# Performance work log

Measured on AMD Instinct MI355X. Metric: run time of the kernel, lower is better.

## Reference

```python
import jax, jax.numpy as jnp
import numpy as np

B, N, K, F_IN, F_OUT = 2, 196608, 9, 64, 64


def setup_inputs() -> dict:
    key = jax.random.key(0)
    k1, k2, k3 = jax.random.split(key, 3)
    x = jax.random.normal(k1, (B, N, F_IN), dtype=jnp.float32)
    adjc = jax.random.randint(k2, (N, K), 0, N, dtype=jnp.int64)
    # first neighbor is the cell itself (typical grid adjacency)
    adjc = adjc.at[:, 0].set(jnp.arange(N, dtype=jnp.int64))
    scale = 1.0 / np.sqrt(K * F_IN)
    W = jax.random.normal(k3, (K, F_IN, F_OUT), dtype=jnp.float32) * scale
    b = jnp.zeros((F_OUT,), dtype=jnp.float32)
    return {"x": x, "adjc": adjc, "W": W, "b": b}


def reference(x, adjc, W, b):
    # get_nh: irregular gather of neighbor features -> [B, N, K, F_in]
    x_nh = x[:, adjc, :]
    # learned layer: contract over (neighborhood, in_features) -> [B, N, F_out]
    out = jnp.einsum("bnkf,kfo->bno", x_nh, W) + b
    return out
```

## Files before the change

kernel.cpp:

```cpp
#include <hip/hip_runtime.h>

#define B_ 2
#define N_ 196608
#define K_ 9
#define F_ 64
#define WROWS 32
#define BROWS 128

typedef __attribute__((ext_vector_type(8))) short short8;
typedef __attribute__((ext_vector_type(4))) unsigned short ushort4v;
typedef __attribute__((ext_vector_type(4))) float f32x4;

__device__ __forceinline__ unsigned short f2bf(float f) {
  unsigned u = __builtin_bit_cast(unsigned, f);
  u = (u + 0x7fffu + ((u >> 16) & 1u)) >> 16;
  return (unsigned short)u;
}

#define XCHUNKS (2L * N_ * 16)
#define XBLK ((int)(XCHUNKS / 256))
__global__ __launch_bounds__(256) void cvt_kernel(const float* __restrict__ x,
                                                  unsigned short* __restrict__ xb,
                                                  const float* __restrict__ W,
                                                  unsigned short* __restrict__ wt) {
  if (blockIdx.x < (unsigned)XBLK) {
    const long i = (long)blockIdx.x * 256 + threadIdx.x;
    const long pn = (long)N_ * 16;
    const int b = (int)(i >= pn);
    const long ci = i - (long)b * pn;
    const long n = ci >> 4;
    const int qd = (int)(ci & 15);
    const float4 v = *(const float4*)(x + ((size_t)b * N_ + n) * F_ + (size_t)qd * 4);
    ushort4v r;
    r[0] = f2bf(v.x); r[1] = f2bf(v.y); r[2] = f2bf(v.z); r[3] = f2bf(v.w);
    *(ushort4v*)(xb + ((size_t)n * 2 + b) * F_ + qd * 4) = r;
  } else {
    const int i = (blockIdx.x - XBLK) * 256 + threadIdx.x;
    const int k = i >> 12;
    const int rem = i & 4095;
    const int o = rem >> 6;
    const int f = rem & 63;
    wt[i] = f2bf(W[(k << 12) + (f << 6) + o]);
  }
}

__global__ __launch_bounds__(256, 2) void nhconv_main(
    const short* __restrict__ xb,
    const int* __restrict__ adjc,
    const short* __restrict__ wt,
    const float* __restrict__ bias,
    float* __restrict__ out) {
  const int tid = (int)threadIdx.x;
  const int w = tid >> 6;
  const int l = tid & 63;
  const int q = l >> 4;
  const int c = l & 15;
  const int n0 = blockIdx.x * BROWS + w * WROWS;

  int aj[2][K_];
#pragma unroll
  for (int rt = 0; rt < 2; ++rt) {
    const int* ap = adjc + (size_t)(n0 + rt * 16 + c) * K_;
#pragma unroll
    for (int k = 0; k < K_; ++k) aj[rt][k] = ap[k];
  }

  short8 ra[2][8], rw[8];
  const short* wbase = wt + q * 8 + (c << 6);

  auto aload = [&](int k, int par) {
#pragma unroll
    for (int p = 0; p < 2; ++p)
#pragma unroll
      for (int fs = 0; fs < 2; ++fs)
#pragma unroll
        for (int rt = 0; rt < 2; ++rt)
          ra[par][p * 4 + fs * 2 + rt] = *(const short8*)(
              xb + ((size_t)(unsigned)aj[rt][k] << 7) + p * 64 + fs * 32 + q * 8);
  };
  auto wload = [&](int k) {
#pragma unroll
    for (int fs = 0; fs < 2; ++fs)
#pragma unroll
      for (int ct = 0; ct < 4; ++ct)
        rw[fs * 4 + ct] = *(const short8*)(wbase + (k << 12) + fs * 32 + (ct << 10));
  };

  f32x4 acc[2][2][4];
#pragma unroll
  for (int p = 0; p < 2; ++p)
#pragma unroll
    for (int rt = 0; rt < 2; ++rt)
#pragma unroll
      for (int ct = 0; ct < 4; ++ct)
        acc[p][rt][ct] = (f32x4){0.f, 0.f, 0.f, 0.f};

  aload(0, 0);

#pragma unroll
  for (int k = 0; k < K_; ++k) {
    if (k > 0) __builtin_amdgcn_s_barrier();
    wload(k);
    if (k + 1 < K_) aload(k + 1, (k + 1) & 1);
    __builtin_amdgcn_sched_barrier(0);

#pragma unroll
    for (int fs = 0; fs < 2; ++fs)
#pragma unroll
      for (int rt = 0; rt < 2; ++rt)
#pragma unroll
        for (int ct = 0; ct < 4; ++ct) {
          const short8 bfr = rw[fs * 4 + ct];
          acc[0][rt][ct] = __builtin_amdgcn_mfma_f32_16x16x32_bf16(
              ra[k & 1][0 + fs * 2 + rt], bfr, acc[0][rt][ct], 0, 0, 0);
          acc[1][rt][ct] = __builtin_amdgcn_mfma_f32_16x16x32_bf16(
              ra[k & 1][4 + fs * 2 + rt], bfr, acc[1][rt][ct], 0, 0, 0);
        }
  }

  float bv[4];
#pragma unroll
  for (int ct = 0; ct < 4; ++ct) bv[ct] = bias[ct * 16 + c];

#pragma unroll
  for (int p = 0; p < 2; ++p) {
    const size_t outbase = ((size_t)p * N_ + (size_t)n0) * F_;
#pragma unroll
    for (int rt = 0; rt < 2; ++rt) {
#pragma unroll
      for (int ct = 0; ct < 4; ++ct) {
#pragma unroll
        for (int rr = 0; rr < 4; ++rr) {
          const int row = rt * 16 + q * 4 + rr;
          __builtin_nontemporal_store(acc[p][rt][ct][rr] + bv[ct],
                                      &out[outbase + (size_t)row * F_ + ct * 16 + c]);
        }
      }
    }
  }
}

extern "C" void kernel_launch(void* const* d_in, const int* in_sizes, int n_in,
                              void* d_out, int out_size, void* d_ws, size_t ws_size,
                              hipStream_t stream) {
  const float* x = (const float*)d_in[0];
  const int* adjc = (const int*)d_in[1];
  const float* W = (const float*)d_in[2];
  const float* bias = (const float*)d_in[3];
  float* out = (float*)d_out;

  unsigned short* xb = (unsigned short*)d_ws;
  unsigned short* wt = (unsigned short*)((char*)d_ws + (size_t)B_ * N_ * F_ * 2);

  cvt_kernel<<<XBLK + 144, 256, 0, stream>>>(x, xb, W, wt);

  nhconv_main<<<N_ / BROWS, 256, 0, stream>>>((const short*)xb, adjc, (const short*)wt,
                                              bias, out);
}
```

Before: 279.7 us.

## Stage weights and adjacency in LDS, deepen gather prefetch, use 512-thread blocks

Each block now copies the full bf16 weight tensor into LDS with an XOR swizzle to avoid bank conflicts, and stages its adjacency rows in LDS. Per-iteration weight fragments are then read from LDS instead of global memory. The gather prefetch goes from double to triple buffering (two steps ahead), the per-iteration s_barrier is removed, and blocks grow to 8 waves covering 256 rows. The aim is to cut repeated global weight traffic and hide gather latency. In exchange, about 83KB of LDS per block and a larger register footprint under the (512,2) launch bound may limit occupancy or cause spills.

```diff
diff --git a/kernel.cpp b/kernel.cpp
--- a/kernel.cpp
+++ b/kernel.cpp
@@ -4,8 +4,10 @@
 #define N_ 196608
 #define K_ 9
 #define F_ 64
+#define WAVES 8
 #define WROWS 32
-#define BROWS 128
+#define BROWS (WAVES * WROWS)
+#define WT16 (K_ * 64 * 8)
 
 typedef __attribute__((ext_vector_type(8))) short short8;
 typedef __attribute__((ext_vector_type(4))) unsigned short ushort4v;
@@ -44,12 +46,15 @@
   }
 }
 
-__global__ __launch_bounds__(256, 2) void nhconv_main(
+__global__ __launch_bounds__(512, 2) void nhconv_main(
     const short* __restrict__ xb,
     const int* __restrict__ adjc,
     const short* __restrict__ wt,
     const float* __restrict__ bias,
     float* __restrict__ out) {
+  __shared__ __align__(16) short lds_wt[WT16 * 8];
+  __shared__ int s_adj[BROWS * K_];
+
   const int tid = (int)threadIdx.x;
   const int w = tid >> 6;
   const int l = tid & 63;
@@ -57,35 +62,39 @@
   const int c = l & 15;
   const int n0 = blockIdx.x * BROWS + w * WROWS;
 
+  {
+    const short8* wt16 = (const short8*)wt;
+    short8* lwt16 = (short8*)lds_wt;
+    for (int g = tid; g < WT16; g += 512) {
+      const int o = (g >> 3) & 63;
+      const int ch = g & 7;
+      lwt16[(g & ~7) | (ch ^ (o & 7))] = wt16[g];
+    }
+  }
+  for (int i = tid; i < BROWS * K_; i += 512)
+    s_adj[i] = __builtin_nontemporal_load(adjc + (size_t)blockIdx.x * BROWS * K_ + i);
+  __syncthreads();
+
   int aj[2][K_];
 #pragma unroll
-  for (int rt = 0; rt < 2; ++rt) {
-    const int* ap = adjc + (size_t)(n0 + rt * 16 + c) * K_;
+  for (int rt = 0; rt < 2; ++rt)
 #pragma unroll
-    for (int k = 0; k < K_; ++k) aj[rt][k] = ap[k];
-  }
+    for (int k = 0; k < K_; ++k)
+      aj[rt][k] = s_adj[(w * WROWS + rt * 16 + c) * K_ + k];
 
-  short8 ra[2][8], rw[8];
-  const short* wbase = wt + q * 8 + (c << 6);
-
-  auto aload = [&](int k, int par) {
+  short8 ra[3][8];
+  auto aload = [&](int k, int set) {
 #pragma unroll
     for (int p = 0; p < 2; ++p)
 #pragma unroll
       for (int fs = 0; fs < 2; ++fs)
 #pragma unroll
         for (int rt = 0; rt < 2; ++rt)
-          ra[par][p * 4 + fs * 2 + rt] = *(const short8*)(
+          ra[set][p * 4 + fs * 2 + rt] = *(const short8*)(
               xb + ((size_t)(unsigned)aj[rt][k] << 7) + p * 64 + fs * 32 + q * 8);
   };
-  auto wload = [&](int k) {
-#pragma unroll
-    for (int fs = 0; fs < 2; ++fs)
-#pragma unroll
-      for (int ct = 0; ct < 4; ++ct)
-        rw[fs * 4 + ct] = *(const short8*)(wbase + (k << 12) + fs * 32 + (ct << 10));
-  };
 
+  const short8* lwt16 = (const short8*)lds_wt;
   f32x4 acc[2][2][4];
 #pragma unroll
   for (int p = 0; p < 2; ++p)
@@ -96,12 +105,18 @@
         acc[p][rt][ct] = (f32x4){0.f, 0.f, 0.f, 0.f};
 
   aload(0, 0);
+  aload(1, 1);
 
 #pragma unroll
   for (int k = 0; k < K_; ++k) {
-    if (k > 0) __builtin_amdgcn_s_barrier();
-    wload(k);
-    if (k + 1 < K_) aload(k + 1, (k + 1) & 1);
+    if (k + 2 < K_) aload(k + 2, (k + 2) % 3);
+    short8 rw[8];
+#pragma unroll
+    for (int fs = 0; fs < 2; ++fs)
+#pragma unroll
+      for (int ct = 0; ct < 4; ++ct)
+        rw[fs * 4 + ct] =
+            lwt16[k * 512 + (ct * 16 + c) * 8 + ((fs * 4 + q) ^ (c & 7))];
     __builtin_amdgcn_sched_barrier(0);
 
 #pragma unroll
@@ -112,9 +127,9 @@
         for (int ct = 0; ct < 4; ++ct) {
           const short8 bfr = rw[fs * 4 + ct];
           acc[0][rt][ct] = __builtin_amdgcn_mfma_f32_16x16x32_bf16(
-              ra[k & 1][0 + fs * 2 + rt], bfr, acc[0][rt][ct], 0, 0, 0);
+              ra[k % 3][0 + fs * 2 + rt], bfr, acc[0][rt][ct], 0, 0, 0);
           acc[1][rt][ct] = __builtin_amdgcn_mfma_f32_16x16x32_bf16(
-              ra[k & 1][4 + fs * 2 + rt], bfr, acc[1][rt][ct], 0, 0, 0);
+              ra[k % 3][4 + fs * 2 + rt], bfr, acc[1][rt][ct], 0, 0, 0);
         }
   }
 
@@ -154,6 +169,6 @@
 
   cvt_kernel<<<XBLK + 144, 256, 0, stream>>>(x, xb, W, wt);
 
-  nhconv_main<<<N_ / BROWS, 256, 0, stream>>>((const short*)xb, adjc, (const short*)wt,
+  nhconv_main<<<N_ / BROWS, 512, 0, stream>>>((const short*)xb, adjc, (const short*)wt,
                                               bias, out);
 }
```

After: 259.7 us. 7.2% less time.
